# Kernel tuning notes

Hardware: AMD Instinct MI355X
Metric: run time of the kernel (lower is better)

The kernel has to match this reference:

```python
import jax, jax.numpy as jnp
import numpy as np

HEADS = 12
ROPE_THETA = 10000.0

def _rope(t):
    # t: [B, H, N, D]; lucidrains interleaved RoPE (rotate_half over adjacent pairs)
    B, H, N, D = t.shape
    inv_freq = 1.0 / (ROPE_THETA ** (jnp.arange(0, D, 2, dtype=jnp.float32) / D))  # [D/2]
    freqs = jnp.arange(N, dtype=jnp.float32)[:, None] * inv_freq[None, :]          # [N, D/2]
    freqs = jnp.repeat(freqs, 2, axis=-1)                                          # [N, D]
    cos, sin = jnp.cos(freqs), jnp.sin(freqs)
    tp = t.reshape(B, H, N, D // 2, 2)
    rot = jnp.stack([-tp[..., 1], tp[..., 0]], axis=-1).reshape(B, H, N, D)
    return t * cos + rot * sin

def setup_inputs() -> dict:
    key = jax.random.key(0)
    k1, k2, k3 = jax.random.split(key, 3)
    dim = 768
    x = jax.random.normal(k1, (2, 2048, dim), dtype=jnp.float32)
    w_qkv = jax.random.normal(k2, (3 * dim, dim), dtype=jnp.float32) * (dim ** -0.5)
    w_proj = jax.random.normal(k3, (dim, dim), dtype=jnp.float32) * (dim ** -0.5)
    b_proj = jnp.zeros((dim,), dtype=jnp.float32)
    return {"x": x, "w_qkv": w_qkv, "w_proj": w_proj, "b_proj": b_proj}

def reference(x, w_qkv, w_proj, b_proj):
    B, N, C = x.shape
    H = HEADS
    d = C // H
    scale = d ** -0.5
    qkv = x @ w_qkv.T                                # [B, N, 3C]
    q, k, v = jnp.split(qkv, 3, axis=-1)
    def to_heads(t):
        return t.reshape(B, N, H, d).transpose(0, 2, 1, 3)  # [B,H,N,d]
    q, k, v = map(to_heads, (q, k, v))
    q = _rope(q * scale)
    k = _rope(k)
    attn = jnp.einsum('bhid,bhjd->bhij', q, k)
    attn = jax.nn.softmax(attn, axis=-1)
    out = jnp.einsum('bhij,bhjd->bhid', attn, v)
    out = out.transpose(0, 2, 1, 3).reshape(B, N, C)
    return out @ w_proj.T + b_proj
```

## Files before the change

kernel.cpp:

```cpp
#include <hip/hip_runtime.h>
#include <math.h>

#define NSEQ 2048
#define CDIM 768
#define NH   12
#define HD   64
#define NB   2

typedef unsigned short u16;
typedef __attribute__((ext_vector_type(8))) short bf16x8;
typedef __attribute__((ext_vector_type(4))) float f32x4;
typedef __attribute__((ext_vector_type(8))) float f32x8;
typedef __attribute__((ext_vector_type(4))) __bf16 bf16x4t;
typedef __attribute__((ext_vector_type(8))) __bf16 bf16x8t;

__device__ __forceinline__ u16 f2bf(float x) {
    unsigned int u = __float_as_uint(x);
    u += 0x7fffu + ((u >> 16) & 1u);
    return (u16)(u >> 16);
}

__device__ __forceinline__ uint4 pack8(float4 a, float4 b) {
    f32x8 v = {a.x, a.y, a.z, a.w, b.x, b.y, b.z, b.w};
    union { bf16x8t t; uint4 u; } o;
    o.t = __builtin_convertvector(v, bf16x8t);
    return o.u;
}

#define LSTR 72

#define GLD16(gp, lp) __builtin_amdgcn_global_load_lds( \
    (__attribute__((address_space(1))) void*)(const void*)(gp), \
    (__attribute__((address_space(3))) void*)(void*)(lp), 16, 0, 0)

__global__ __launch_bounds__(256)
void qkv_mfma_kernel(const float* __restrict__ Xf, const float* __restrict__ Wf,
                     u16* __restrict__ Qb, u16* __restrict__ Kb,
                     u16* __restrict__ Vb)
{
    __shared__ __align__(16) u16 S[2 * 128 * LSTR];
    u16* As = S;
    u16* Bs = S + 128 * LSTR;

    const int tid  = threadIdx.x;
    const int lane = tid & 63;
    const int wid  = tid >> 6;
    const int l15  = lane & 15;
    const int quad = lane >> 4;
    const int wr = wid >> 1, wc = wid & 1;
    const int m0 = blockIdx.x * 128;
    const int n0 = blockIdx.y * 128;

    const int row = tid >> 3, c8s = (tid & 7) << 3;

    f32x4 acc[4][4];
#pragma unroll
    for (int mi = 0; mi < 4; ++mi)
#pragma unroll
        for (int ni = 0; ni < 4; ++ni)
            acc[mi][ni] = (f32x4){0.f, 0.f, 0.f, 0.f};

    float4 pa[4][2], pb[4][2];
#pragma unroll
    for (int it = 0; it < 4; ++it) {
        size_t ga = (size_t)(m0 + row + 32 * it) * CDIM + c8s;
        size_t gb = (size_t)(n0 + row + 32 * it) * CDIM + c8s;
        pa[it][0] = *(const float4*)&Xf[ga];
        pa[it][1] = *(const float4*)&Xf[ga + 4];
        pb[it][0] = *(const float4*)&Wf[gb];
        pb[it][1] = *(const float4*)&Wf[gb + 4];
    }

    for (int kt = 0; kt < CDIM; kt += 64) {
        __syncthreads();
#pragma unroll
        for (int it = 0; it < 4; ++it) {
            *(uint4*)&As[(row + 32 * it) * LSTR + c8s] =
                pack8(pa[it][0], pa[it][1]);
            *(uint4*)&Bs[(row + 32 * it) * LSTR + c8s] =
                pack8(pb[it][0], pb[it][1]);
        }
        __syncthreads();

        if (kt + 64 < CDIM) {
#pragma unroll
            for (int it = 0; it < 4; ++it) {
                size_t ga = (size_t)(m0 + row + 32 * it) * CDIM + kt + 64 + c8s;
                size_t gb = (size_t)(n0 + row + 32 * it) * CDIM + kt + 64 + c8s;
                pa[it][0] = *(const float4*)&Xf[ga];
                pa[it][1] = *(const float4*)&Xf[ga + 4];
                pb[it][0] = *(const float4*)&Wf[gb];
                pb[it][1] = *(const float4*)&Wf[gb + 4];
            }
        }

#pragma unroll
        for (int k = 0; k < 2; ++k) {
            bf16x8 af[4];
#pragma unroll
            for (int mi = 0; mi < 4; ++mi)
                af[mi] = *(const bf16x8*)
                    &As[(wr * 64 + mi * 16 + l15) * LSTR + quad * 8 + 32 * k];
#pragma unroll
            for (int ni = 0; ni < 4; ++ni) {
                bf16x8 bfr = *(const bf16x8*)
                    &Bs[(wc * 64 + ni * 16 + l15) * LSTR + quad * 8 + 32 * k];
#pragma unroll
                for (int mi = 0; mi < 4; ++mi)
                    acc[mi][ni] = __builtin_amdgcn_mfma_f32_16x16x32_bf16(
                        af[mi], bfr, acc[mi][ni], 0, 0, 0);
            }
        }
    }

    __syncthreads();

    const int bi      = m0 >> 11;
    const int nbase   = (m0 & 2047) + wr * 64;
    const int colbase = n0 + wc * 64;
    const int sel     = colbase / CDIM;
    const int h       = (colbase % CDIM) >> 6;

    u16* Ew = S + wid * 64 * LSTR;
    const int grow = lane >> 3;
    const int gc8  = (lane & 7) << 3;

    if (sel == 2) {
#pragma unroll
        for (int ni = 0; ni < 4; ++ni)
#pragma unroll
            for (int mi = 0; mi < 4; ++mi)
#pragma unroll
                for (int r = 0; r < 4; ++r)
                    Ew[(ni * 16 + l15) * LSTR + mi * 16 + quad * 4 + r] =
                        f2bf(acc[mi][ni][r]);
        u16* dst = Vb + (size_t)(bi * NH + h) * HD * NSEQ;
#pragma unroll
        for (int it = 0; it < 8; ++it) {
            int dd = grow + 8 * it;
            *(uint4*)&dst[(size_t)dd * NSEQ + nbase + gc8] =
                *(const uint4*)&Ew[dd * LSTR + gc8];
        }
    } else {
        u16* dst = ((sel == 0) ? Qb : Kb) + (size_t)(bi * NH + h) * NSEQ * HD;
        const float scl = (sel == 0) ? 0.125f : 1.0f;
#pragma unroll
        for (int ni = 0; ni < 4; ++ni) {
            int dd = ni * 16 + l15;
            float invf = expf(-0.14391156831212787f * (float)(dd & ~1));
#pragma unroll
            for (int mi = 0; mi < 4; ++mi) {
                f32x4 val = acc[mi][ni];
#pragma unroll
                for (int r = 0; r < 4; ++r) {
                    float e = val[r] * scl;
                    float p = __shfl_xor(e, 1);
                    int n = nbase + mi * 16 + quad * 4 + r;
                    float sv, cv;
                    __sincosf((float)n * invf, &sv, &cv);
                    float o = (dd & 1) ? (e * cv + p * sv)
                                       : (e * cv - p * sv);
                    Ew[(mi * 16 + quad * 4 + r) * LSTR + dd] = f2bf(o);
                }
            }
        }
#pragma unroll
        for (int it = 0; it < 8; ++it) {
            int tr = grow + 8 * it;
            *(uint4*)&dst[(size_t)(nbase + tr) * HD + gc8] =
                *(const uint4*)&Ew[tr * LSTR + gc8];
        }
    }
}

#define STAGE_KV(BUF, kt_) do {                                               \
    GLD16(Kg + ((size_t)(((kt_) << 6) + r0) * HD + cs),                       \
          &Ks[BUF][wid * 512]);                                               \
    GLD16(Kg + ((size_t)(((kt_) << 6) + r0 + 32) * HD + cs),                  \
          &Ks[BUF][wid * 512 + 2048]);                                        \
    GLD16(Vg + ((size_t)r0 * NSEQ + ((kt_) << 6) + cs),                       \
          &Vs[BUF][wid * 512]);                                               \
    GLD16(Vg + ((size_t)(r0 + 32) * NSEQ + ((kt_) << 6) + cs),                \
          &Vs[BUF][wid * 512 + 2048]);                                        \
} while (0)

#define ATTN_STEP(kt_, CUR, NXT) do {                                         \
    if ((kt_) + 1 < NSEQ / 64) STAGE_KV(NXT, (kt_) + 1);                      \
    f32x4 sacc[4];                                                            \
    _Pragma("unroll")                                                         \
    for (int mt = 0; mt < 4; ++mt) sacc[mt] = (f32x4){0.f, 0.f, 0.f, 0.f};    \
    _Pragma("unroll")                                                         \
    for (int k = 0; k < 2; ++k) {                                             \
        _Pragma("unroll")                                                     \
        for (int mt = 0; mt < 4; ++mt) {                                      \
            bf16x8 ak = *(const bf16x8*)                                      \
                &Ks[CUR][(mt * 16 + l15) * 64 + ((quad * 8 + 32 * k) ^ swz)]; \
            sacc[mt] = __builtin_amdgcn_mfma_f32_16x16x32_bf16(               \
                ak, aq[k], sacc[mt], 0, 0, 0);                                \
        }                                                                     \
    }                                                                         \
    _Pragma("unroll")                                                         \
    for (int mt = 0; mt < 4; ++mt) {                                          \
        f32x4 ev;                                                             \
        _Pragma("unroll")                                                     \
        for (int r = 0; r < 4; ++r) ev[r] = __expf(sacc[mt][r]);              \
        bf16x4t pbk = __builtin_convertvector(ev, bf16x4t);                   \
        *(bf16x4t*)&Pw[l15 * 64 + ((mt * 16 + quad * 4) ^ swz)] = pbk;        \
    }                                                                         \
    _Pragma("unroll")                                                         \
    for (int k = 0; k < 2; ++k) {                                             \
        bf16x8 ap = *(const bf16x8*)                                          \
            &Pw[l15 * 64 + ((quad * 8 + 32 * k) ^ swz)];                      \
        lacc = __builtin_amdgcn_mfma_f32_16x16x32_bf16(                       \
            ap, vone, lacc, 0, 0, 0);                                         \
        _Pragma("unroll")                                                     \
        for (int t = 0; t < 4; ++t) {                                         \
            bf16x8 bv = *(const bf16x8*)                                      \
                &Vs[CUR][(t * 16 + l15) * 64 + ((quad * 8 + 32 * k) ^ swz)];  \
            O[t] = __builtin_amdgcn_mfma_f32_16x16x32_bf16(                   \
                ap, bv, O[t], 0, 0, 0);                                       \
        }                                                                     \
    }                                                                         \
    __syncthreads();                                                          \
} while (0)

__global__ __launch_bounds__(256)
void attn_kernel(const u16* __restrict__ Qb, const u16* __restrict__ Kb,
                 const u16* __restrict__ Vt, u16* __restrict__ AO)
{
    __shared__ __align__(16) u16 Ks[2][64 * 64];
    __shared__ __align__(16) u16 Vs[2][64 * 64];
    __shared__ __align__(16) u16 Ps[4][16 * 64];

    const int tid  = threadIdx.x;
    const int lane = tid & 63;
    const int wid  = tid >> 6;
    const int l15  = lane & 15;
    const int quad = lane >> 4;
    const int swz  = (l15 & 7) << 3;
    const int qt = blockIdx.x;
    const int bh = blockIdx.y;

    const u16* Qg = Qb + ((size_t)bh * NSEQ + qt * 64) * HD;
    const u16* Kg = Kb + (size_t)bh * NSEQ * HD;
    const u16* Vg = Vt + (size_t)bh * HD * NSEQ;

    const int r0 = tid >> 3;
    const int cs = ((tid & 7) ^ (r0 & 7)) << 3;

    bf16x8 aq[2];
    aq[0] = *(const bf16x8*)&Qg[(wid * 16 + l15) * HD + quad * 8];
    aq[1] = *(const bf16x8*)&Qg[(wid * 16 + l15) * HD + quad * 8 + 32];

    union { u16 s[8]; bf16x8 v; } oneu;
#pragma unroll
    for (int i = 0; i < 8; ++i) oneu.s[i] = 0x3f80;
    const bf16x8 vone = oneu.v;

    f32x4 O[4];
#pragma unroll
    for (int t = 0; t < 4; ++t) O[t] = (f32x4){0.f, 0.f, 0.f, 0.f};
    f32x4 lacc = (f32x4){0.f, 0.f, 0.f, 0.f};

    u16* Pw = Ps[wid];

    STAGE_KV(0, 0);
    __syncthreads();

    for (int kt = 0; kt < NSEQ / 64; kt += 2) {
        ATTN_STEP(kt, 0, 1);
        ATTN_STEP(kt + 1, 1, 0);
    }

    float inv4[4];
#pragma unroll
    for (int r = 0; r < 4; ++r) inv4[r] = 1.0f / lacc[r];

    const int b = bh / NH, h = bh % NH;
#pragma unroll
    for (int r = 0; r < 4; ++r) {
        size_t row = (size_t)b * NSEQ + qt * 64 + wid * 16 + quad * 4 + r;
#pragma unroll
        for (int t = 0; t < 4; ++t)
            AO[row * CDIM + h * HD + t * 16 + l15] = f2bf(O[t][r] * inv4[r]);
    }
}

__global__ __launch_bounds__(256)
void proj_kernel(const u16* __restrict__ A, const float* __restrict__ Wf,
                 const float* __restrict__ bias, float* __restrict__ out)
{
    __shared__ __align__(16) u16 As[64 * 64];
    __shared__ __align__(16) u16 Bs[64 * 64];
    const int tid  = threadIdx.x;
    const int lane = tid & 63;
    const int wid  = tid >> 6;
    const int l15  = lane & 15;
    const int quad = lane >> 4;
    const int swz  = (l15 & 7) << 3;
    const int wr = wid >> 1, wc = wid & 1;
    const int m0 = blockIdx.x * 64;
    const int n0 = blockIdx.y * 64;

    const int r0 = tid >> 3;
    const int cs = ((tid & 7) ^ (r0 & 7)) << 3;
    const int c8 = (tid & 7) << 3;
    const int bswz = c8 ^ ((r0 & 7) << 3);

    f32x4 acc[2][2];
#pragma unroll
    for (int mi = 0; mi < 2; ++mi)
#pragma unroll
        for (int ni = 0; ni < 2; ++ni)
            acc[mi][ni] = (f32x4){0.f, 0.f, 0.f, 0.f};

    for (int kt = 0; kt < CDIM; kt += 64) {
        __syncthreads();
        GLD16(A + ((size_t)(m0 + r0) * CDIM + kt + cs),      &As[wid * 512]);
        GLD16(A + ((size_t)(m0 + r0 + 32) * CDIM + kt + cs), &As[wid * 512 + 2048]);
        {
            size_t gb0 = (size_t)(n0 + r0) * CDIM + kt + c8;
            size_t gb1 = (size_t)(n0 + r0 + 32) * CDIM + kt + c8;
            float4 w0 = *(const float4*)&Wf[gb0];
            float4 w1 = *(const float4*)&Wf[gb0 + 4];
            float4 w2 = *(const float4*)&Wf[gb1];
            float4 w3 = *(const float4*)&Wf[gb1 + 4];
            *(uint4*)&Bs[r0 * 64 + bswz]        = pack8(w0, w1);
            *(uint4*)&Bs[(r0 + 32) * 64 + bswz] = pack8(w2, w3);
        }
        __syncthreads();

#pragma unroll
        for (int k = 0; k < 2; ++k) {
            bf16x8 af[2], bf[2];
#pragma unroll
            for (int mi = 0; mi < 2; ++mi)
                af[mi] = *(const bf16x8*)
                    &As[(wr * 32 + mi * 16 + l15) * 64 + ((quad * 8 + 32 * k) ^ swz)];
#pragma unroll
            for (int ni = 0; ni < 2; ++ni)
                bf[ni] = *(const bf16x8*)
                    &Bs[(wc * 32 + ni * 16 + l15) * 64 + ((quad * 8 + 32 * k) ^ swz)];
#pragma unroll
            for (int mi = 0; mi < 2; ++mi)
#pragma unroll
                for (int ni = 0; ni < 2; ++ni)
                    acc[mi][ni] = __builtin_amdgcn_mfma_f32_16x16x32_bf16(
                        af[mi], bf[ni], acc[mi][ni], 0, 0, 0);
        }
    }

#pragma unroll
    for (int ni = 0; ni < 2; ++ni) {
        int col = n0 + wc * 32 + ni * 16 + l15;
        float bb = bias[col];
#pragma unroll
        for (int mi = 0; mi < 2; ++mi) {
            int row = m0 + wr * 32 + mi * 16 + quad * 4;
#pragma unroll
            for (int r = 0; r < 4; ++r)
                out[(size_t)(row + r) * CDIM + col] = acc[mi][ni][r] + bb;
        }
    }
}

extern "C" void kernel_launch(void* const* d_in, const int* in_sizes, int n_in,
                              void* d_out, int out_size, void* d_ws,
                              size_t ws_size, hipStream_t stream)
{
    const float* X     = (const float*)d_in[0];
    const float* Wqkv  = (const float*)d_in[1];
    const float* Wproj = (const float*)d_in[2];
    const float* bias  = (const float*)d_in[3];
    float* out = (float*)d_out;

    const size_t per_buf = (size_t)NB * NH * NSEQ * HD;
    u16* Qb  = (u16*)d_ws;
    u16* Kb  = Qb + per_buf;
    u16* Vb  = Kb + per_buf;
    u16* AOb = Vb + per_buf;

    qkv_mfma_kernel<<<dim3(32, 18), 256, 0, stream>>>(X, Wqkv, Qb, Kb, Vb);
    attn_kernel<<<dim3(32, 24), 256, 0, stream>>>(Qb, Kb, Vb, AOb);
    proj_kernel<<<dim3(64, 12), 256, 0, stream>>>(AOb, Wproj, bias, out);
}
```

Measured before the change: 161.6 us.

## Remap blocks for XCD locality, double-buffer QKV LDS, load attention K/V from global

The three kernels switch to 1D grids with a remapping intended to place blocks that share inputs on the same XCD, for better L2 reuse. The QKV GEMM gains a double-buffered LDS stage, so it needs one barrier per k-step instead of two. The attention kernel drops LDS staging of K/V and has each wave load its K and V fragments directly from global memory, and it wraps the MFMA runs in s_setprio. Together these aim to cut barrier count and LDS traffic, at the cost of more redundant global/L2 reads of K/V per block and a doubled LDS footprint in the GEMM.

```diff
diff --git a/kernel.cpp b/kernel.cpp
--- a/kernel.cpp
+++ b/kernel.cpp
@@ -38,9 +38,7 @@
                      u16* __restrict__ Qb, u16* __restrict__ Kb,
                      u16* __restrict__ Vb)
 {
-    __shared__ __align__(16) u16 S[2 * 128 * LSTR];
-    u16* As = S;
-    u16* Bs = S + 128 * LSTR;
+    __shared__ __align__(16) u16 S[4 * 128 * LSTR];
 
     const int tid  = threadIdx.x;
     const int lane = tid & 63;
@@ -48,8 +46,11 @@
     const int l15  = lane & 15;
     const int quad = lane >> 4;
     const int wr = wid >> 1, wc = wid & 1;
-    const int m0 = blockIdx.x * 128;
-    const int n0 = blockIdx.y * 128;
+
+    const int f   = blockIdx.x;
+    const int L   = (f & 7) * 72 + (f >> 3);
+    const int m0  = (L & 31) * 128;
+    const int n0  = (L >> 5) * 128;
 
     const int row = tid >> 3, c8s = (tid & 7) << 3;
 
@@ -71,8 +72,9 @@
         pb[it][1] = *(const float4*)&Wf[gb + 4];
     }
 
-    for (int kt = 0; kt < CDIM; kt += 64) {
-        __syncthreads();
+    {
+        u16* As = S;
+        u16* Bs = S + 128 * LSTR;
 #pragma unroll
         for (int it = 0; it < 4; ++it) {
             *(uint4*)&As[(row + 32 * it) * LSTR + c8s] =
@@ -80,9 +82,16 @@
             *(uint4*)&Bs[(row + 32 * it) * LSTR + c8s] =
                 pack8(pb[it][0], pb[it][1]);
         }
-        __syncthreads();
-
-        if (kt + 64 < CDIM) {
+    }
+    __syncthreads();
+
+    int cur = 0;
+    for (int kt = 0; kt < CDIM; kt += 64) {
+        const u16* Ac = S + cur * (2 * 128 * LSTR);
+        const u16* Bc = Ac + 128 * LSTR;
+        const bool more = (kt + 64 < CDIM);
+
+        if (more) {
 #pragma unroll
             for (int it = 0; it < 4; ++it) {
                 size_t ga = (size_t)(m0 + row + 32 * it) * CDIM + kt + 64 + c8s;
@@ -100,20 +109,32 @@
 #pragma unroll
             for (int mi = 0; mi < 4; ++mi)
                 af[mi] = *(const bf16x8*)
-                    &As[(wr * 64 + mi * 16 + l15) * LSTR + quad * 8 + 32 * k];
+                    &Ac[(wr * 64 + mi * 16 + l15) * LSTR + quad * 8 + 32 * k];
 #pragma unroll
             for (int ni = 0; ni < 4; ++ni) {
                 bf16x8 bfr = *(const bf16x8*)
-                    &Bs[(wc * 64 + ni * 16 + l15) * LSTR + quad * 8 + 32 * k];
+                    &Bc[(wc * 64 + ni * 16 + l15) * LSTR + quad * 8 + 32 * k];
 #pragma unroll
                 for (int mi = 0; mi < 4; ++mi)
                     acc[mi][ni] = __builtin_amdgcn_mfma_f32_16x16x32_bf16(
                         af[mi], bfr, acc[mi][ni], 0, 0, 0);
             }
         }
-    }
-
-    __syncthreads();
+
+        if (more) {
+            u16* An = S + (cur ^ 1) * (2 * 128 * LSTR);
+            u16* Bn = An + 128 * LSTR;
+#pragma unroll
+            for (int it = 0; it < 4; ++it) {
+                *(uint4*)&An[(row + 32 * it) * LSTR + c8s] =
+                    pack8(pa[it][0], pa[it][1]);
+                *(uint4*)&Bn[(row + 32 * it) * LSTR + c8s] =
+                    pack8(pb[it][0], pb[it][1]);
+            }
+        }
+        __syncthreads();
+        cur ^= 1;
+    }
 
     const int bi      = m0 >> 11;
     const int nbase   = (m0 & 2047) + wr * 64;
@@ -173,63 +194,10 @@
     }
 }
 
-#define STAGE_KV(BUF, kt_) do {                                               \
-    GLD16(Kg + ((size_t)(((kt_) << 6) + r0) * HD + cs),                       \
-          &Ks[BUF][wid * 512]);                                               \
-    GLD16(Kg + ((size_t)(((kt_) << 6) + r0 + 32) * HD + cs),                  \
-          &Ks[BUF][wid * 512 + 2048]);                                        \
-    GLD16(Vg + ((size_t)r0 * NSEQ + ((kt_) << 6) + cs),                       \
-          &Vs[BUF][wid * 512]);                                               \
-    GLD16(Vg + ((size_t)(r0 + 32) * NSEQ + ((kt_) << 6) + cs),                \
-          &Vs[BUF][wid * 512 + 2048]);                                        \
-} while (0)
-
-#define ATTN_STEP(kt_, CUR, NXT) do {                                         \
-    if ((kt_) + 1 < NSEQ / 64) STAGE_KV(NXT, (kt_) + 1);                      \
-    f32x4 sacc[4];                                                            \
-    _Pragma("unroll")                                                         \
-    for (int mt = 0; mt < 4; ++mt) sacc[mt] = (f32x4){0.f, 0.f, 0.f, 0.f};    \
-    _Pragma("unroll")                                                         \
-    for (int k = 0; k < 2; ++k) {                                             \
-        _Pragma("unroll")                                                     \
-        for (int mt = 0; mt < 4; ++mt) {                                      \
-            bf16x8 ak = *(const bf16x8*)                                      \
-                &Ks[CUR][(mt * 16 + l15) * 64 + ((quad * 8 + 32 * k) ^ swz)]; \
-            sacc[mt] = __builtin_amdgcn_mfma_f32_16x16x32_bf16(               \
-                ak, aq[k], sacc[mt], 0, 0, 0);                                \
-        }                                                                     \
-    }                                                                         \
-    _Pragma("unroll")                                                         \
-    for (int mt = 0; mt < 4; ++mt) {                                          \
-        f32x4 ev;                                                             \
-        _Pragma("unroll")                                                     \
-        for (int r = 0; r < 4; ++r) ev[r] = __expf(sacc[mt][r]);              \
-        bf16x4t pbk = __builtin_convertvector(ev, bf16x4t);                   \
-        *(bf16x4t*)&Pw[l15 * 64 + ((mt * 16 + quad * 4) ^ swz)] = pbk;        \
-    }                                                                         \
-    _Pragma("unroll")                                                         \
-    for (int k = 0; k < 2; ++k) {                                             \
-        bf16x8 ap = *(const bf16x8*)                                          \
-            &Pw[l15 * 64 + ((quad * 8 + 32 * k) ^ swz)];                      \
-        lacc = __builtin_amdgcn_mfma_f32_16x16x32_bf16(                       \
-            ap, vone, lacc, 0, 0, 0);                                         \
-        _Pragma("unroll")                                                     \
-        for (int t = 0; t < 4; ++t) {                                         \
-            bf16x8 bv = *(const bf16x8*)                                      \
-                &Vs[CUR][(t * 16 + l15) * 64 + ((quad * 8 + 32 * k) ^ swz)];  \
-            O[t] = __builtin_amdgcn_mfma_f32_16x16x32_bf16(                   \
-                ap, bv, O[t], 0, 0, 0);                                       \
-        }                                                                     \
-    }                                                                         \
-    __syncthreads();                                                          \
-} while (0)
-
 __global__ __launch_bounds__(256)
 void attn_kernel(const u16* __restrict__ Qb, const u16* __restrict__ Kb,
                  const u16* __restrict__ Vt, u16* __restrict__ AO)
 {
-    __shared__ __align__(16) u16 Ks[2][64 * 64];
-    __shared__ __align__(16) u16 Vs[2][64 * 64];
     __shared__ __align__(16) u16 Ps[4][16 * 64];
 
     const int tid  = threadIdx.x;
@@ -238,23 +206,23 @@
     const int l15  = lane & 15;
     const int quad = lane >> 4;
     const int swz  = (l15 & 7) << 3;
-    const int qt = blockIdx.x;
-    const int bh = blockIdx.y;
+
+    const int f  = blockIdx.x;
+    const int i  = f >> 3;
+    const int bh = (f & 7) * 3 + (i >> 5);
+    const int qt = i & 31;
 
     const u16* Qg = Qb + ((size_t)bh * NSEQ + qt * 64) * HD;
     const u16* Kg = Kb + (size_t)bh * NSEQ * HD;
     const u16* Vg = Vt + (size_t)bh * HD * NSEQ;
 
-    const int r0 = tid >> 3;
-    const int cs = ((tid & 7) ^ (r0 & 7)) << 3;
-
     bf16x8 aq[2];
     aq[0] = *(const bf16x8*)&Qg[(wid * 16 + l15) * HD + quad * 8];
     aq[1] = *(const bf16x8*)&Qg[(wid * 16 + l15) * HD + quad * 8 + 32];
 
     union { u16 s[8]; bf16x8 v; } oneu;
 #pragma unroll
-    for (int i = 0; i < 8; ++i) oneu.s[i] = 0x3f80;
+    for (int ii = 0; ii < 8; ++ii) oneu.s[ii] = 0x3f80;
     const bf16x8 vone = oneu.v;
 
     f32x4 O[4];
@@ -264,12 +232,59 @@
 
     u16* Pw = Ps[wid];
 
-    STAGE_KV(0, 0);
-    __syncthreads();
-
-    for (int kt = 0; kt < NSEQ / 64; kt += 2) {
-        ATTN_STEP(kt, 0, 1);
-        ATTN_STEP(kt + 1, 1, 0);
+    for (int kt = 0; kt < NSEQ / 64; ++kt) {
+        const u16* Kt = Kg + (size_t)(kt << 6) * HD;
+        const u16* Vp = Vg + (kt << 6);
+
+        bf16x8 ak0[4], ak1[4], bv0[4], bv1[4];
+#pragma unroll
+        for (int mt = 0; mt < 4; ++mt) {
+            ak0[mt] = *(const bf16x8*)&Kt[(mt * 16 + l15) * HD + quad * 8];
+            ak1[mt] = *(const bf16x8*)&Kt[(mt * 16 + l15) * HD + quad * 8 + 32];
+        }
+#pragma unroll
+        for (int t = 0; t < 4; ++t) {
+            bv0[t] = *(const bf16x8*)&Vp[(size_t)(t * 16 + l15) * NSEQ + quad * 8];
+            bv1[t] = *(const bf16x8*)&Vp[(size_t)(t * 16 + l15) * NSEQ + quad * 8 + 32];
+        }
+
+        f32x4 sacc[4];
+#pragma unroll
+        for (int mt = 0; mt < 4; ++mt) sacc[mt] = (f32x4){0.f, 0.f, 0.f, 0.f};
+        __builtin_amdgcn_s_setprio(1);
+#pragma unroll
+        for (int mt = 0; mt < 4; ++mt)
+            sacc[mt] = __builtin_amdgcn_mfma_f32_16x16x32_bf16(
+                ak0[mt], aq[0], sacc[mt], 0, 0, 0);
+#pragma unroll
+        for (int mt = 0; mt < 4; ++mt)
+            sacc[mt] = __builtin_amdgcn_mfma_f32_16x16x32_bf16(
+                ak1[mt], aq[1], sacc[mt], 0, 0, 0);
+        __builtin_amdgcn_s_setprio(0);
+
+#pragma unroll
+        for (int mt = 0; mt < 4; ++mt) {
+            f32x4 ev;
+#pragma unroll
+            for (int r = 0; r < 4; ++r) ev[r] = __expf(sacc[mt][r]);
+            bf16x4t pbk = __builtin_convertvector(ev, bf16x4t);
+            *(bf16x4t*)&Pw[l15 * 64 + ((mt * 16 + quad * 4) ^ swz)] = pbk;
+        }
+        bf16x8 ap0 = *(const bf16x8*)&Pw[l15 * 64 + ((quad * 8) ^ swz)];
+        bf16x8 ap1 = *(const bf16x8*)&Pw[l15 * 64 + ((quad * 8 + 32) ^ swz)];
+
+        __builtin_amdgcn_s_setprio(1);
+        lacc = __builtin_amdgcn_mfma_f32_16x16x32_bf16(ap0, vone, lacc, 0, 0, 0);
+#pragma unroll
+        for (int t = 0; t < 4; ++t)
+            O[t] = __builtin_amdgcn_mfma_f32_16x16x32_bf16(
+                ap0, bv0[t], O[t], 0, 0, 0);
+        lacc = __builtin_amdgcn_mfma_f32_16x16x32_bf16(ap1, vone, lacc, 0, 0, 0);
+#pragma unroll
+        for (int t = 0; t < 4; ++t)
+            O[t] = __builtin_amdgcn_mfma_f32_16x16x32_bf16(
+                ap1, bv1[t], O[t], 0, 0, 0);
+        __builtin_amdgcn_s_setprio(0);
     }
 
     float inv4[4];
@@ -279,10 +294,10 @@
     const int b = bh / NH, h = bh % NH;
 #pragma unroll
     for (int r = 0; r < 4; ++r) {
-        size_t row = (size_t)b * NSEQ + qt * 64 + wid * 16 + quad * 4 + r;
+        size_t orow = (size_t)b * NSEQ + qt * 64 + wid * 16 + quad * 4 + r;
 #pragma unroll
         for (int t = 0; t < 4; ++t)
-            AO[row * CDIM + h * HD + t * 16 + l15] = f2bf(O[t][r] * inv4[r]);
+            AO[orow * CDIM + h * HD + t * 16 + l15] = f2bf(O[t][r] * inv4[r]);
     }
 }
 
@@ -299,8 +314,11 @@
     const int quad = lane >> 4;
     const int swz  = (l15 & 7) << 3;
     const int wr = wid >> 1, wc = wid & 1;
-    const int m0 = blockIdx.x * 64;
-    const int n0 = blockIdx.y * 64;
+
+    const int fb = blockIdx.x;
+    const int L  = (fb & 7) * 96 + (fb >> 3);
+    const int m0 = (L & 63) * 64;
+    const int n0 = (L >> 6) * 64;
 
     const int r0 = tid >> 3;
     const int cs = ((tid & 7) ^ (r0 & 7)) << 3;
@@ -356,10 +374,10 @@
         float bb = bias[col];
 #pragma unroll
         for (int mi = 0; mi < 2; ++mi) {
-            int row = m0 + wr * 32 + mi * 16 + quad * 4;
+            int rw = m0 + wr * 32 + mi * 16 + quad * 4;
 #pragma unroll
             for (int r = 0; r < 4; ++r)
-                out[(size_t)(row + r) * CDIM + col] = acc[mi][ni][r] + bb;
+                out[(size_t)(rw + r) * CDIM + col] = acc[mi][ni][r] + bb;
         }
     }
 }
@@ -380,7 +398,7 @@
     u16* Vb  = Kb + per_buf;
     u16* AOb = Vb + per_buf;
 
-    qkv_mfma_kernel<<<dim3(32, 18), 256, 0, stream>>>(X, Wqkv, Qb, Kb, Vb);
-    attn_kernel<<<dim3(32, 24), 256, 0, stream>>>(Qb, Kb, Vb, AOb);
-    proj_kernel<<<dim3(64, 12), 256, 0, stream>>>(AOb, Wproj, bias, out);
-}
+    qkv_mfma_kernel<<<dim3(576), 256, 0, stream>>>(X, Wqkv, Qb, Kb, Vb);
+    attn_kernel<<<dim3(768), 256, 0, stream>>>(Qb, Kb, Vb, AOb);
+    proj_kernel<<<dim3(768), 256, 0, stream>>>(AOb, Wproj, bias, out);
+}
```

After: 294.6 us. 82.4% more time.
